# Kernel optimization log

Measured on AMD Instinct MI355X. Metric: run time of the kernel, lower is better.

## Reference

```python
import jax, jax.numpy as jnp
import numpy as np

N_USERS = 100_000
N_ITEMS = 50_000
N_NODES = N_USERS + N_ITEMS
D = 64
K = 32          # n_intents
N_LAYERS = 2
E_UI = 1_000_000
E_UU = 500_000
E_II = 500_000


def spmm(row, col, val, x, n_rows):
    # sparse[n_rows, :] @ x via gather + segment_sum  (torch_sparse.spmm)
    return jax.ops.segment_sum(val[:, None] * x[col], row, num_segments=n_rows)


def row_normalize(row, val, n_rows):
    # D^-1 * values, matching normalization_indices_values / embed21 row scaling
    s = jax.ops.segment_sum(val, row, num_segments=n_rows)
    inv = jnp.where(s != 0, 1.0 / s, 0.0)
    return inv[row] * val


def l2norm(x):
    # F.normalize(x) along dim=1
    return x / jnp.maximum(jnp.linalg.norm(x, axis=1, keepdims=True), 1e-12)


def setup_inputs():
    key = jax.random.key(0)
    ks = jax.random.split(key, 16)
    return dict(
        user_emb=0.1 * jax.random.normal(ks[0], (N_USERS, D), jnp.float32),
        item_emb=0.1 * jax.random.normal(ks[1], (N_ITEMS, D), jnp.float32),
        intents=0.1 * jax.random.normal(ks[2], (D, K), jnp.float32),
        W2=0.1 * jax.random.normal(ks[3], (4 * D, D), jnp.float32),
        b2=jnp.zeros((D,), jnp.float32),
        uu_w=jax.random.uniform(ks[4], (E_UU,), jnp.float32),
        ii_w=jax.random.uniform(ks[5], (E_II,), jnp.float32),
        ui_u=jax.random.randint(ks[6], (E_UI,), 0, N_USERS),
        ui_i=jax.random.randint(ks[7], (E_UI,), 0, N_ITEMS),
        uu_h=jax.random.randint(ks[8], (E_UU,), 0, N_USERS),
        uu_t=jax.random.randint(ks[9], (E_UU,), 0, N_USERS),
        ii_h=jax.random.randint(ks[10], (E_II,), 0, N_ITEMS),
        ii_t=jax.random.randint(ks[11], (E_II,), 0, N_ITEMS),
    )


def reference(user_emb, item_emb, intents, W2, b2, uu_w, ii_w,
              ui_u, ui_i, uu_h, uu_t, ii_h, ii_t):
    # symmetric bipartite adjacency: (u -> n_users+i) and (n_users+i -> u)
    all_h = jnp.concatenate([ui_u, ui_i + N_USERS])
    all_t = jnp.concatenate([ui_i + N_USERS, ui_u])

    # _cal_sparse_adj: G = D^-1/2 A D^-1/2 on edge values
    deg = jax.ops.segment_sum(jnp.ones((2 * E_UI,), jnp.float32), all_h,
                              num_segments=N_NODES)
    d_inv = jnp.where(deg > 0, deg ** -0.5, 0.0)
    G_val = d_inv[all_h] * d_inv[all_t]

    # normalization_indices_values for UU / II weighted graphs (D^-1 * w)
    uu_val = row_normalize(uu_h, uu_w, N_USERS)
    ii_val = row_normalize(ii_h, ii_w, N_ITEMS)

    def embed11(x):
        return spmm(all_h, all_t, G_val, x, N_NODES)

    def embed12(x):
        u, i = x[:N_USERS], x[N_USERS:]
        return jnp.concatenate([spmm(uu_h, uu_t, uu_val, u, N_USERS),
                                spmm(ii_h, ii_t, ii_val, i, N_ITEMS)], axis=0)

    def intent_edge_weights(h_emb, t_emb, head_idx, n_heads):
        # per-edge intent distribution + alpha-weighted node aggregation
        dist = jax.nn.softmax((h_emb * t_emb) @ intents, axis=1)   # [E, K]
        alpha = (jnp.sum(h_emb * t_emb, axis=1) + 1.0) / 2.0        # [E]
        agg = jax.ops.segment_sum(alpha[:, None] * dist, head_idx,
                                  num_segments=n_heads)             # [n, K]
        recip = jnp.where(agg != 0, 1.0 / agg, 0.0)
        edge_int = alpha[:, None] * recip[head_idx]                 # [E, K]
        return jnp.mean(dist * edge_int, axis=1)                    # [E]

    def embed21(feature, x):
        h = feature[ui_u]               # [E_UI, D]
        t = feature[ui_i + N_USERS]     # [E_UI, D]
        w_u = intent_edge_weights(h, t, ui_u, N_USERS)
        w_i = intent_edge_weights(h, t, ui_i, N_ITEMS)
        w = row_normalize(all_h, jnp.concatenate([w_u, w_i]), N_NODES)
        return l2norm(spmm(all_h, all_t, w, x, N_NODES))

    def embed22(feature, x):
        uf, itf = feature[:N_USERS], feature[N_USERS:]
        ux, ix = x[:N_USERS], x[N_USERS:]
        w_uu = intent_edge_weights(uf[uu_h], uf[uu_t], uu_h, N_USERS)
        w_uu = row_normalize(uu_h, w_uu, N_USERS)
        w_ii = intent_edge_weights(itf[ii_h], itf[ii_t], ii_h, N_ITEMS)
        w_ii = row_normalize(ii_h, w_ii, N_ITEMS)
        return l2norm(jnp.concatenate([spmm(uu_h, uu_t, w_uu, ux, N_USERS),
                                       spmm(ii_h, ii_t, w_ii, ix, N_ITEMS)], axis=0))

    x = jnp.concatenate([user_emb, item_emb], axis=0)
    acc = x
    for _ in range(N_LAYERS):
        g1 = embed11(x)
        g2 = embed12(x)
        t1 = embed21(x, x)
        t2 = embed22(x, x)
        # mlp2 fusion (eval mode, dropout off): sigmoid gate over 4-way concat
        gate = jax.nn.sigmoid(jnp.concatenate([g1, g2, t1, t2], axis=1) @ W2 + b2)
        x = gate * (g1 + g2) + (1.0 - gate) * (t1 + t2)
        acc = acc + x
    return acc
```

## Files before the change

kernel.cpp:

```cpp
#include <hip/hip_runtime.h>
#include <hip/hip_fp16.h>

#define NU 100000
#define NI 50000
#define NN 150000
#define DD 64
#define KK 32
#define EUI 1000000
#define EUU 500000
#define EII 500000
#define ROWS_PB 64

static inline int cdiv(long a, int b) { return (int)((a + b - 1) / b); }

__device__ __forceinline__ float rdlane(float v, int l) {
    return __int_as_float(__builtin_amdgcn_readlane(__float_as_int(v), l));
}


__global__ void k_count(const int* __restrict__ h, int* __restrict__ cnt, int E) {
    int e = blockIdx.x * blockDim.x + threadIdx.x;
    if (e < E) atomicAdd(&cnt[h[e]], 1);
}

__global__ __launch_bounds__(1024) void k_scan(const int* __restrict__ cnt,
                                               int* __restrict__ rp, int n) {
    __shared__ int wsum[16];
    __shared__ int carry_s;
    int tid = threadIdx.x;
    int lane = tid & 63, wid = tid >> 6;
    if (tid == 0) carry_s = 0;
    __syncthreads();
    for (int base = 0; base < n; base += 1024) {
        int i = base + tid;
        int v = (i < n) ? cnt[i] : 0;
        int s = v;
#pragma unroll
        for (int off = 1; off < 64; off <<= 1) {
            int t = __shfl_up(s, off, 64);
            if (lane >= off) s += t;
        }
        if (lane == 63) wsum[wid] = s;
        __syncthreads();
        int woff = 0, total = 0;
#pragma unroll
        for (int w = 0; w < 16; w++) { int ws = wsum[w]; total += ws; if (w < wid) woff += ws; }
        int carry = carry_s;
        if (i < n) rp[i] = carry + woff + (s - v);
        __syncthreads();
        if (tid == 0) carry_s = carry + total;
        __syncthreads();
    }
    if (tid == 0) rp[n] = carry_s;
}

__global__ void k_scatter(const int* __restrict__ h, const int* __restrict__ rp,
                          int* __restrict__ cur, int* __restrict__ lst, int E) {
    int e = blockIdx.x * blockDim.x + threadIdx.x;
    if (e >= E) return;
    int r = h[e];
    int p = rp[r] + atomicAdd(&cur[r], 1);
    lst[p] = e;
}

__global__ void k_dinv(const int* __restrict__ rpu, const int* __restrict__ rpi,
                       float* __restrict__ dinv) {
    int t = blockIdx.x * blockDim.x + threadIdx.x;
    if (t >= NN) return;
    int deg = (t < NU) ? rpu[t + 1] - rpu[t] : rpi[t - NU + 1] - rpi[t - NU];
    dinv[t] = deg > 0 ? rsqrtf((float)deg) : 0.0f;
}

__global__ void k_rowsum_inv(const int* __restrict__ rp, const int* __restrict__ lst,
                             const float* __restrict__ w, float* __restrict__ out, int n) {
    int r = blockIdx.x * blockDim.x + threadIdx.x;
    if (r >= n) return;
    float s = 0.f;
    int e1 = rp[r + 1];
    for (int e = rp[r]; e < e1; e++) s += w[lst[e]];
    out[r] = (s != 0.0f) ? 1.0f / s : 0.0f;
}

__global__ void k_wdiff(const float* __restrict__ W2, float* __restrict__ Wd_g,
                        float* __restrict__ Wd_t) {
    int i = blockIdx.x * blockDim.x + threadIdx.x;
    if (i >= DD * DD) return;
    Wd_g[i] = W2[i] - W2[DD * DD + i];
    Wd_t[i] = W2[2 * DD * DD + i] - W2[3 * DD * DD + i];
}

__global__ void k_init(const float* __restrict__ ue, const float* __restrict__ ie,
                       __half* __restrict__ xh, float* __restrict__ acc) {
    size_t i = (size_t)blockIdx.x * blockDim.x + threadIdx.x;
    if (i >= (size_t)NN * DD) return;
    float v = (i < (size_t)NU * DD) ? ue[i] : ie[i - (size_t)NU * DD];
    xh[i] = __float2half(v);
    acc[i] = v;
}


__global__ void k_posU(const int* __restrict__ lst, int* __restrict__ pos, int E) {
    int p = blockIdx.x * blockDim.x + threadIdx.x;
    if (p < E) pos[lst[p]] = p;
}

__global__ void k_mapUI(const int* __restrict__ lst_i, const int* __restrict__ posU,
                        int* __restrict__ mUI, int E) {
    int p = blockIdx.x * blockDim.x + threadIdx.x;
    if (p < E) mUI[p] = posU[lst_i[p]];
}

__global__ void k_build_ui(const int* __restrict__ lst_u, const int* __restrict__ ui_u,
                           const int* __restrict__ ui_i, int* __restrict__ headU,
                           int* __restrict__ colUI, int E) {
    int p = blockIdx.x * blockDim.x + threadIdx.x;
    if (p >= E) return;
    int e = lst_u[p];
    headU[p] = ui_u[e];
    colUI[p] = ui_i[e] + NU;
}

__global__ void k_build_colI(const int* __restrict__ lst_i, const int* __restrict__ ui_u,
                             int* __restrict__ colUI, int E) {
    int p = blockIdx.x * blockDim.x + threadIdx.x;
    if (p < E) colUI[EUI + p] = ui_u[lst_i[p]];
}

__global__ void k_build_rp2(const int* __restrict__ rp_u, const int* __restrict__ rp_i,
                            const int* __restrict__ rp_uu, const int* __restrict__ rp_ii,
                            int* __restrict__ rp_ui, int* __restrict__ rp_s) {
    int t = blockIdx.x * blockDim.x + threadIdx.x;
    if (t > NN) return;
    rp_ui[t] = (t <= NU) ? rp_u[t] : rp_i[t - NU] + EUI;
    rp_s[t]  = (t <= NU) ? rp_uu[t] : rp_ii[t - NU] + EUU;
}

__global__ void k_build_gw(const int* __restrict__ rp, const int* __restrict__ col,
                           const float* __restrict__ dinv, float* __restrict__ gw, int n) {
    int r = blockIdx.x * blockDim.x + threadIdx.x;
    if (r >= n) return;
    float dh = dinv[r];
    int e1 = rp[r + 1];
    for (int p = rp[r]; p < e1; p++) gw[p] = dh * dinv[col[p]];
}

__global__ void k_build_s(const int* __restrict__ lst, const int* __restrict__ eh,
                          const int* __restrict__ et, const float* __restrict__ ew,
                          const float* __restrict__ inv, int off, int peo,
                          int* __restrict__ head, int* __restrict__ col,
                          float* __restrict__ bw, int E) {
    int p = blockIdx.x * blockDim.x + threadIdx.x;
    if (p >= E) return;
    int e = lst[p];
    int h = eh[e];
    head[peo + p] = h + off;
    col[peo + p] = et[e] + off;
    bw[peo + p] = ew[e] * inv[h];
}


__global__ __launch_bounds__(256) void k_passA(
        const int* __restrict__ head, const int* __restrict__ col,
        const __half* __restrict__ x, const float* __restrict__ intents,
        __half* __restrict__ c_out, int E) {
    __shared__ float Wl[DD * KK];
    for (int idx = threadIdx.x; idx < DD * KK; idx += blockDim.x) Wl[idx] = intents[idx];
    __syncthreads();
    int stride = gridDim.x * blockDim.x;
    for (int p = blockIdx.x * blockDim.x + threadIdx.x; p < E; p += stride) {
        const uint4* hp = (const uint4*)(x + (size_t)head[p] * DD);
        const uint4* tp = (const uint4*)(x + (size_t)col[p] * DD);
        uint4 hraw[8], traw[8];
#pragma unroll
        for (int j = 0; j < 8; j++) hraw[j] = hp[j];
#pragma unroll
        for (int j = 0; j < 8; j++) traw[j] = tp[j];
        const __half2* h2 = (const __half2*)hraw;
        const __half2* t2 = (const __half2*)traw;
        float logit[KK];
#pragma unroll
        for (int k = 0; k < KK; k++) logit[k] = 0.f;
        float dot = 0.f;
#pragma unroll 4
        for (int l4 = 0; l4 < 16; l4++) {
            float2 ha = __half22float2(h2[2 * l4]), hb = __half22float2(h2[2 * l4 + 1]);
            float2 ta = __half22float2(t2[2 * l4]), tb = __half22float2(t2[2 * l4 + 1]);
            float p0 = ha.x * ta.x, p1 = ha.y * ta.y, p2 = hb.x * tb.x, p3 = hb.y * tb.y;
            dot += p0 + p1 + p2 + p3;
            const float* w = &Wl[l4 * 4 * KK];
#pragma unroll
            for (int k = 0; k < KK; k++)
                logit[k] += p0 * w[k] + p1 * w[KK + k] + p2 * w[2 * KK + k] + p3 * w[3 * KK + k];
        }
        float m = logit[0];
#pragma unroll
        for (int k = 1; k < KK; k++) m = fmaxf(m, logit[k]);
        float ssum = 0.f;
#pragma unroll
        for (int k = 0; k < KK; k++) { float ev = __expf(logit[k] - m); logit[k] = ev; ssum += ev; }
        float scale = 0.5f * (dot + 1.0f) / ssum;
        uint4 pk[4];
        unsigned int* u = (unsigned int*)pk;
#pragma unroll
        for (int k2 = 0; k2 < 16; k2++) {
            __half2 hh = __floats2half2_rn(logit[2 * k2] * scale, logit[2 * k2 + 1] * scale);
            u[k2] = *reinterpret_cast<const unsigned int*>(&hh);
        }
        uint4* dst = (uint4*)(c_out + (size_t)p * KK);
#pragma unroll
        for (int q = 0; q < 4; q++) dst[q] = pk[q];
    }
}

#define PRD(a0, a1, a2, a3, l) \
    rdlane(((l) & 3) == 0 ? (a0) : ((l) & 3) == 1 ? (a1) : ((l) & 3) == 2 ? (a2) : (a3), (l) >> 2)

__global__ __launch_bounds__(512) void k_fused_ui(
        const int* __restrict__ rp, const int* __restrict__ col,
        const float* __restrict__ gw, const __half* __restrict__ cbuf,
        const int* __restrict__ mUI,
        const float* __restrict__ Wd_g, const float* __restrict__ Wd_t,
        const float* __restrict__ b2, const __half* __restrict__ x,
        __half* __restrict__ gs, __half* __restrict__ ts,
        float* __restrict__ zp, int nrows) {
    __shared__ float Wg[DD * DD];
    __shared__ float Wt[DD * DD];
    for (int i = threadIdx.x; i < DD * DD; i += 512) { Wg[i] = Wd_g[i]; Wt[i] = Wd_t[i]; }
    __syncthreads();
    int wid = threadIdx.x >> 6, lane = threadIdx.x & 63;
    int sub = lane & 15, grp = lane >> 4;
    float b2v = b2[lane];
    const uint2* xq = (const uint2*)x;
    const unsigned int* cu = (const unsigned int*)cbuf;
    int rbase = blockIdx.x * ROWS_PB + wid * 8;
    for (int rr = 0; rr < 8; rr++) {
        int r = rbase + rr;
        if (r >= nrows) break;
        bool item = (r >= NU);
        int e0 = rp[r], e1 = rp[r + 1];
        float a0 = 0.f, a1 = 0.f;
        for (int e = e0; e < e1; e += 4) {
            int idx = e + grp;
            if (idx < e1) {
                int ci = item ? mUI[idx - EUI] : idx;
                unsigned int cv = cu[(size_t)ci * 16 + sub];
                float2 cf = __half22float2(*(const __half2*)&cv);
                a0 += cf.x; a1 += cf.y;
            }
        }
        a0 += __shfl_xor(a0, 16, 64); a0 += __shfl_xor(a0, 32, 64);
        a1 += __shfl_xor(a1, 16, 64); a1 += __shfl_xor(a1, 32, 64);
        float2 rc;
        rc.x = (a0 != 0.f) ? 1.f / a0 : 0.f;
        rc.y = (a1 != 0.f) ? 1.f / a1 : 0.f;
        float g0 = 0, g1 = 0, g2 = 0, g3 = 0, t0 = 0, t1 = 0, t2 = 0, t3 = 0;
        float rsacc = 0.f;
        int e = e0;
        for (; e + 8 <= e1; e += 8) {
#pragma unroll
            for (int u = 0; u < 2; u++) {
                int idx = e + 4 * u + grp;
                int cc = col[idx];
                float wg = gw[idx];
                int ci = item ? mUI[idx - EUI] : idx;
                unsigned int cv = cu[(size_t)ci * 16 + sub];
                float2 cf = __half22float2(*(const __half2*)&cv);
                float pd = fmaf(cf.x, rc.x, cf.y * rc.y);
                pd += __shfl_xor(pd, 1, 64); pd += __shfl_xor(pd, 2, 64);
                pd += __shfl_xor(pd, 4, 64); pd += __shfl_xor(pd, 8, 64);
                float wt = pd * (1.0f / KK);
                rsacc += wt;
                uint2 raw = xq[(size_t)cc * 16 + sub];
                float2 xa = __half22float2(*(const __half2*)&raw.x);
                float2 xb = __half22float2(*(const __half2*)&raw.y);
                g0 += wg * xa.x; g1 += wg * xa.y; g2 += wg * xb.x; g3 += wg * xb.y;
                t0 += wt * xa.x; t1 += wt * xa.y; t2 += wt * xb.x; t3 += wt * xb.y;
            }
        }
        for (; e < e1; e += 4) {
            int idx = e + grp;
            if (idx < e1) {
                int cc = col[idx];
                float wg = gw[idx];
                int ci = item ? mUI[idx - EUI] : idx;
                unsigned int cv = cu[(size_t)ci * 16 + sub];
                float2 cf = __half22float2(*(const __half2*)&cv);
                float pd = fmaf(cf.x, rc.x, cf.y * rc.y);
                pd += __shfl_xor(pd, 1, 64); pd += __shfl_xor(pd, 2, 64);
                pd += __shfl_xor(pd, 4, 64); pd += __shfl_xor(pd, 8, 64);
                float wt = pd * (1.0f / KK);
                rsacc += wt;
                uint2 raw = xq[(size_t)cc * 16 + sub];
                float2 xa = __half22float2(*(const __half2*)&raw.x);
                float2 xb = __half22float2(*(const __half2*)&raw.y);
                g0 += wg * xa.x; g1 += wg * xa.y; g2 += wg * xb.x; g3 += wg * xb.y;
                t0 += wt * xa.x; t1 += wt * xa.y; t2 += wt * xb.x; t3 += wt * xb.y;
            }
        }
#pragma unroll
        for (int off = 16; off <= 32; off <<= 1) {
            g0 += __shfl_xor(g0, off, 64); g1 += __shfl_xor(g1, off, 64);
            g2 += __shfl_xor(g2, off, 64); g3 += __shfl_xor(g3, off, 64);
            t0 += __shfl_xor(t0, off, 64); t1 += __shfl_xor(t1, off, 64);
            t2 += __shfl_xor(t2, off, 64); t3 += __shfl_xor(t3, off, 64);
            rsacc += __shfl_xor(rsacc, off, 64);
        }
        float rsv = (rsacc != 0.f) ? 1.0f / rsacc : 0.f;
        t0 *= rsv; t1 *= rsv; t2 *= rsv; t3 *= rsv;
        float ss = t0 * t0 + t1 * t1 + t2 * t2 + t3 * t3;
        ss += __shfl_xor(ss, 1, 64); ss += __shfl_xor(ss, 2, 64);
        ss += __shfl_xor(ss, 4, 64); ss += __shfl_xor(ss, 8, 64);
        float inv_n = 1.0f / fmaxf(sqrtf(ss), 1e-12f);
        t0 *= inv_n; t1 *= inv_n; t2 *= inv_n; t3 *= inv_n;
        float zv = b2v;
#pragma unroll
        for (int l = 0; l < DD; l++) {
            float gl = PRD(g0, g1, g2, g3, l);
            float tl = PRD(t0, t1, t2, t3, l);
            zv += gl * Wg[l * DD + lane] + tl * Wt[l * DD + lane];
        }
        float ga0 = __shfl(g0, lane >> 2, 64), ga1 = __shfl(g1, lane >> 2, 64);
        float ga2 = __shfl(g2, lane >> 2, 64), ga3 = __shfl(g3, lane >> 2, 64);
        float ta0 = __shfl(t0, lane >> 2, 64), ta1 = __shfl(t1, lane >> 2, 64);
        float ta2 = __shfl(t2, lane >> 2, 64), ta3 = __shfl(t3, lane >> 2, 64);
        int j = lane & 3;
        float gsv = j == 0 ? ga0 : j == 1 ? ga1 : j == 2 ? ga2 : ga3;
        float tsv = j == 0 ? ta0 : j == 1 ? ta1 : j == 2 ? ta2 : ta3;
        size_t oi = (size_t)r * DD + lane;
        gs[oi] = __float2half(gsv);
        ts[oi] = __float2half(tsv);
        zp[oi] = zv;
    }
}

__global__ __launch_bounds__(512) void k_fused_fin(
        const int* __restrict__ rp, const int* __restrict__ col,
        const float* __restrict__ bw, const __half* __restrict__ cbuf,
        const float* __restrict__ W1, const float* __restrict__ W3,
        const __half* __restrict__ x, const __half* __restrict__ gs,
        const __half* __restrict__ ts, const float* __restrict__ zp,
        __half* __restrict__ xh_out, float* __restrict__ acc, int nrows) {
    __shared__ float Wa[DD * DD];
    __shared__ float Wb[DD * DD];
    for (int i = threadIdx.x; i < DD * DD; i += 512) { Wa[i] = W1[i]; Wb[i] = W3[i]; }
    __syncthreads();
    int wid = threadIdx.x >> 6, lane = threadIdx.x & 63;
    int sub = lane & 15, grp = lane >> 4;
    const uint2* xq = (const uint2*)x;
    const unsigned int* cu = (const unsigned int*)cbuf;
    int rbase = blockIdx.x * ROWS_PB + wid * 8;
    for (int rr = 0; rr < 8; rr++) {
        int r = rbase + rr;
        if (r >= nrows) break;
        int e0 = rp[r], e1 = rp[r + 1];
        float a0 = 0.f, a1 = 0.f;
        for (int e = e0; e < e1; e += 4) {
            int idx = e + grp;
            if (idx < e1) {
                unsigned int cv = cu[(size_t)idx * 16 + sub];
                float2 cf = __half22float2(*(const __half2*)&cv);
                a0 += cf.x; a1 += cf.y;
            }
        }
        a0 += __shfl_xor(a0, 16, 64); a0 += __shfl_xor(a0, 32, 64);
        a1 += __shfl_xor(a1, 16, 64); a1 += __shfl_xor(a1, 32, 64);
        float2 rc;
        rc.x = (a0 != 0.f) ? 1.f / a0 : 0.f;
        rc.y = (a1 != 0.f) ? 1.f / a1 : 0.f;
        float g0 = 0, g1 = 0, g2 = 0, g3 = 0, t0 = 0, t1 = 0, t2 = 0, t3 = 0;
        float rsacc = 0.f;
        int e = e0;
        for (; e + 8 <= e1; e += 8) {
#pragma unroll
            for (int u = 0; u < 2; u++) {
                int idx = e + 4 * u + grp;
                int cc = col[idx];
                float wg = bw[idx];
                unsigned int cv = cu[(size_t)idx * 16 + sub];
                float2 cf = __half22float2(*(const __half2*)&cv);
                float pd = fmaf(cf.x, rc.x, cf.y * rc.y);
                pd += __shfl_xor(pd, 1, 64); pd += __shfl_xor(pd, 2, 64);
                pd += __shfl_xor(pd, 4, 64); pd += __shfl_xor(pd, 8, 64);
                float wt = pd * (1.0f / KK);
                rsacc += wt;
                uint2 raw = xq[(size_t)cc * 16 + sub];
                float2 xa = __half22float2(*(const __half2*)&raw.x);
                float2 xb = __half22float2(*(const __half2*)&raw.y);
                g0 += wg * xa.x; g1 += wg * xa.y; g2 += wg * xb.x; g3 += wg * xb.y;
                t0 += wt * xa.x; t1 += wt * xa.y; t2 += wt * xb.x; t3 += wt * xb.y;
            }
        }
        for (; e < e1; e += 4) {
            int idx = e + grp;
            if (idx < e1) {
                int cc = col[idx];
                float wg = bw[idx];
                unsigned int cv = cu[(size_t)idx * 16 + sub];
                float2 cf = __half22float2(*(const __half2*)&cv);
                float pd = fmaf(cf.x, rc.x, cf.y * rc.y);
                pd += __shfl_xor(pd, 1, 64); pd += __shfl_xor(pd, 2, 64);
                pd += __shfl_xor(pd, 4, 64); pd += __shfl_xor(pd, 8, 64);
                float wt = pd * (1.0f / KK);
                rsacc += wt;
                uint2 raw = xq[(size_t)cc * 16 + sub];
                float2 xa = __half22float2(*(const __half2*)&raw.x);
                float2 xb = __half22float2(*(const __half2*)&raw.y);
                g0 += wg * xa.x; g1 += wg * xa.y; g2 += wg * xb.x; g3 += wg * xb.y;
                t0 += wt * xa.x; t1 += wt * xa.y; t2 += wt * xb.x; t3 += wt * xb.y;
            }
        }
#pragma unroll
        for (int off = 16; off <= 32; off <<= 1) {
            g0 += __shfl_xor(g0, off, 64); g1 += __shfl_xor(g1, off, 64);
            g2 += __shfl_xor(g2, off, 64); g3 += __shfl_xor(g3, off, 64);
            t0 += __shfl_xor(t0, off, 64); t1 += __shfl_xor(t1, off, 64);
            t2 += __shfl_xor(t2, off, 64); t3 += __shfl_xor(t3, off, 64);
            rsacc += __shfl_xor(rsacc, off, 64);
        }
        float rsv = (rsacc != 0.f) ? 1.0f / rsacc : 0.f;
        t0 *= rsv; t1 *= rsv; t2 *= rsv; t3 *= rsv;
        float ss = t0 * t0 + t1 * t1 + t2 * t2 + t3 * t3;
        ss += __shfl_xor(ss, 1, 64); ss += __shfl_xor(ss, 2, 64);
        ss += __shfl_xor(ss, 4, 64); ss += __shfl_xor(ss, 8, 64);
        float inv_n = 1.0f / fmaxf(sqrtf(ss), 1e-12f);
        t0 *= inv_n; t1 *= inv_n; t2 *= inv_n; t3 *= inv_n;
        uint2 gp2 = ((const uint2*)(gs + (size_t)r * DD))[sub];
        uint2 tp2 = ((const uint2*)(ts + (size_t)r * DD))[sub];
        float2 gpa = __half22float2(*(const __half2*)&gp2.x);
        float2 gpb = __half22float2(*(const __half2*)&gp2.y);
        float2 tpa = __half22float2(*(const __half2*)&tp2.x);
        float2 tpb = __half22float2(*(const __half2*)&tp2.y);
        float gf0 = gpa.x + g0, gf1 = gpa.y + g1, gf2 = gpb.x + g2, gf3 = gpb.y + g3;
        float tf0 = tpa.x + t0, tf1 = tpa.y + t1, tf2 = tpb.x + t2, tf3 = tpb.y + t3;
        size_t oi = (size_t)r * DD + lane;
        float zv = zp[oi];
#pragma unroll
        for (int l = 0; l < DD; l++) {
            float gl = PRD(gf0, gf1, gf2, gf3, l);
            float tl = PRD(tf0, tf1, tf2, tf3, l);
            zv += gl * Wa[l * DD + lane] + tl * Wb[l * DD + lane];
        }
        float ga0 = __shfl(gf0, lane >> 2, 64), ga1 = __shfl(gf1, lane >> 2, 64);
        float ga2 = __shfl(gf2, lane >> 2, 64), ga3 = __shfl(gf3, lane >> 2, 64);
        float ta0 = __shfl(tf0, lane >> 2, 64), ta1 = __shfl(tf1, lane >> 2, 64);
        float ta2 = __shfl(tf2, lane >> 2, 64), ta3 = __shfl(tf3, lane >> 2, 64);
        int j = lane & 3;
        float gfin = j == 0 ? ga0 : j == 1 ? ga1 : j == 2 ? ga2 : ga3;
        float tfin = j == 0 ? ta0 : j == 1 ? ta1 : j == 2 ? ta2 : ta3;
        float gate = 1.0f / (1.0f + __expf(-zv));
        float xn = gate * gfin + (1.0f - gate) * tfin;
        xh_out[oi] = __float2half(xn);
        acc[oi] += xn;
    }
}


extern "C" void kernel_launch(void* const* d_in, const int* in_sizes, int n_in,
                              void* d_out, int out_size, void* d_ws, size_t ws_size,
                              hipStream_t stream) {
    const float* user_emb = (const float*)d_in[0];
    const float* item_emb = (const float*)d_in[1];
    const float* intents  = (const float*)d_in[2];
    const float* W2       = (const float*)d_in[3];
    const float* b2       = (const float*)d_in[4];
    const float* uu_w     = (const float*)d_in[5];
    const float* ii_w     = (const float*)d_in[6];
    const int*   ui_u     = (const int*)d_in[7];
    const int*   ui_i     = (const int*)d_in[8];
    const int*   uu_h     = (const int*)d_in[9];
    const int*   uu_t     = (const int*)d_in[10];
    const int*   ii_h     = (const int*)d_in[11];
    const int*   ii_t     = (const int*)d_in[12];
    float* acc = (float*)d_out;

    char* pw = (char*)d_ws;
    auto allocb = [&](size_t nbytes) -> char* {
        char* r = pw;
        pw += (nbytes + 255) & ~(size_t)255;
        return r;
    };
    __half* gs   = (__half*)allocb((size_t)NN * DD * 2);
    __half* ts   = (__half*)allocb((size_t)NN * DD * 2);
    float* zp    = (float*)allocb((size_t)NN * DD * 4);
    __half* xh0  = (__half*)allocb((size_t)NN * DD * 2);
    __half* xh1  = (__half*)allocb((size_t)NN * DD * 2);
    __half* c    = (__half*)allocb((size_t)EUI * KK * 2);
    float* dinv  = (float*)allocb((size_t)NN * 4);
    float* iuu   = (float*)allocb((size_t)NU * 4);
    float* iii   = (float*)allocb((size_t)NI * 4);
    float* Wd_g  = (float*)allocb((size_t)DD * DD * 4);
    float* Wd_t  = (float*)allocb((size_t)DD * DD * 4);
    int* rp_u    = (int*)allocb(((size_t)NU + 1) * 4);
    int* rp_i    = (int*)allocb(((size_t)NI + 1) * 4);
    int* rp_uu   = (int*)allocb(((size_t)NU + 1) * 4);
    int* rp_ii   = (int*)allocb(((size_t)NI + 1) * 4);
    int* rp_ui   = (int*)allocb(((size_t)NN + 1) * 4);
    int* rp_s    = (int*)allocb(((size_t)NN + 1) * 4);
    int* headU   = (int*)allocb((size_t)EUI * 4);
    int* colUI   = (int*)allocb((size_t)2 * EUI * 4);
    int* head_s  = (int*)allocb((size_t)(EUU + EII) * 4);
    int* col_s   = (int*)allocb((size_t)(EUU + EII) * 4);
    float* bw_s  = (float*)allocb((size_t)(EUU + EII) * 4);
    int* mUI     = (int*)allocb((size_t)EUI * 4);
    float* gwUI  = (float*)allocb((size_t)2 * EUI * 4);

    char* ca = (char*)c;
    int* cur    = (int*)ca;  ca += ((size_t)NU * 4 + 255) & ~(size_t)255;
    int* lst_u  = (int*)ca;  ca += ((size_t)EUI * 4 + 255) & ~(size_t)255;
    int* lst_i  = (int*)ca;  ca += ((size_t)EUI * 4 + 255) & ~(size_t)255;
    int* lst_uu = (int*)ca;  ca += ((size_t)EUU * 4 + 255) & ~(size_t)255;
    int* lst_ii = (int*)ca;  ca += ((size_t)EII * 4 + 255) & ~(size_t)255;
    int* posU   = (int*)ca;

    const int B = 256;

    auto build_csr = [&](const int* h, int E, int n, int* rp, int* lst) {
        hipMemsetAsync(cur, 0, (size_t)n * 4, stream);
        k_count<<<cdiv(E, B), B, 0, stream>>>(h, cur, E);
        k_scan<<<1, 1024, 0, stream>>>(cur, rp, n);
        hipMemsetAsync(cur, 0, (size_t)n * 4, stream);
        k_scatter<<<cdiv(E, B), B, 0, stream>>>(h, rp, cur, lst, E);
    };

    build_csr(ui_u, EUI, NU, rp_u, lst_u);
    build_csr(ui_i, EUI, NI, rp_i, lst_i);
    build_csr(uu_h, EUU, NU, rp_uu, lst_uu);
    build_csr(ii_h, EII, NI, rp_ii, lst_ii);
    k_dinv<<<cdiv(NN, B), B, 0, stream>>>(rp_u, rp_i, dinv);
    k_rowsum_inv<<<cdiv(NU, B), B, 0, stream>>>(rp_uu, lst_uu, uu_w, iuu, NU);
    k_rowsum_inv<<<cdiv(NI, B), B, 0, stream>>>(rp_ii, lst_ii, ii_w, iii, NI);
    k_build_rp2<<<cdiv(NN + 1, B), B, 0, stream>>>(rp_u, rp_i, rp_uu, rp_ii, rp_ui, rp_s);
    k_build_ui<<<cdiv(EUI, B), B, 0, stream>>>(lst_u, ui_u, ui_i, headU, colUI, EUI);
    k_build_colI<<<cdiv(EUI, B), B, 0, stream>>>(lst_i, ui_u, colUI, EUI);
    k_posU<<<cdiv(EUI, B), B, 0, stream>>>(lst_u, posU, EUI);
    k_mapUI<<<cdiv(EUI, B), B, 0, stream>>>(lst_i, posU, mUI, EUI);
    k_build_s<<<cdiv(EUU, B), B, 0, stream>>>(lst_uu, uu_h, uu_t, uu_w, iuu, 0, 0,
                                              head_s, col_s, bw_s, EUU);
    k_build_s<<<cdiv(EII, B), B, 0, stream>>>(lst_ii, ii_h, ii_t, ii_w, iii, NU, EUU,
                                              head_s, col_s, bw_s, EII);
    k_build_gw<<<cdiv(NN, B), B, 0, stream>>>(rp_ui, colUI, dinv, gwUI, NN);
    k_wdiff<<<cdiv(DD * DD, B), B, 0, stream>>>(W2, Wd_g, Wd_t);
    k_init<<<cdiv((long)NN * DD, B), B, 0, stream>>>(user_emb, item_emb, xh0, acc);

    for (int layer = 0; layer < 2; ++layer) {
        const __half* xin = (layer == 0) ? xh0 : xh1;
        __half* xout = (layer == 0) ? xh1 : xh0;

        k_passA<<<1024, B, 0, stream>>>(headU, colUI, xin, intents, c, EUI);
        k_fused_ui<<<cdiv(NN, ROWS_PB), 512, 0, stream>>>(rp_ui, colUI, gwUI, c, mUI,
                                                          Wd_g, Wd_t, b2, xin, gs, ts, zp, NN);

        k_passA<<<1024, B, 0, stream>>>(head_s, col_s, xin, intents, c, EUU + EII);
        k_fused_fin<<<cdiv(NN, ROWS_PB), 512, 0, stream>>>(rp_s, col_s, bw_s, c,
                                                           W2 + DD * DD, W2 + 3 * DD * DD,
                                                           xin, gs, ts, zp, xout, acc, NN);
    }
}
```

Before: 2.201 ms.

## Bucket edges by tail-node shard so passA gathers hit a localized x range

Adds a one-time counting sort that reorders each edge list into 8 shards by tail column range, with the original position kept for the output write. passA then assigns blocks to shards round-robin (blockIdx&7), so concurrently running blocks gather tail rows from a narrower slice of x, aiming for better L2/MALL locality on the random gathers. The cost is extra preprocessing kernels, extra index arrays, and scattered writes of the c output through tpos.

```diff
diff --git a/kernel.cpp b/kernel.cpp
--- a/kernel.cpp
+++ b/kernel.cpp
@@ -10,11 +10,17 @@
 #define EUU 500000
 #define EII 500000
 #define ROWS_PB 64
+#define NB_UI ((EUI + 255) / 256)
+#define NB_S ((EUU + EII + 255) / 256)
 
 static inline int cdiv(long a, int b) { return (int)((a + b - 1) / b); }
 
 __device__ __forceinline__ float rdlane(float v, int l) {
     return __int_as_float(__builtin_amdgcn_readlane(__float_as_int(v), l));
+}
+
+__device__ __forceinline__ int shard_of(int col) {
+    return (col < NU) ? col / 12500 : (col - NU) / 6250;
 }
 
 
@@ -159,17 +165,66 @@
 }
 
 
-__global__ __launch_bounds__(256) void k_passA(
+__global__ __launch_bounds__(256) void k_cntmat(const int* __restrict__ col,
+                                                int* __restrict__ cntmat, int NB, int E) {
+    __shared__ int lc[8];
+    if (threadIdx.x < 8) lc[threadIdx.x] = 0;
+    __syncthreads();
+    int p = blockIdx.x * 256 + threadIdx.x;
+    if (p < E) atomicAdd(&lc[shard_of(col[p])], 1);
+    __syncthreads();
+    if (threadIdx.x < 8) cntmat[threadIdx.x * NB + blockIdx.x] = lc[threadIdx.x];
+}
+
+__global__ __launch_bounds__(256) void k_scatmat(
         const int* __restrict__ head, const int* __restrict__ col,
+        const int* __restrict__ sc, int NB, int E,
+        int* __restrict__ head2, int* __restrict__ col2, int* __restrict__ tpos) {
+    __shared__ int sbase[8];
+    __shared__ int wcnt[4][8];
+    int tid = threadIdx.x, lane = tid & 63, w = tid >> 6;
+    if (tid < 8) sbase[tid] = sc[tid * NB + blockIdx.x];
+    int p = blockIdx.x * 256 + tid;
+    int sh = -1, h = 0, c = 0;
+    if (p < E) { h = head[p]; c = col[p]; sh = shard_of(c); }
+    int rank = 0;
+#pragma unroll
+    for (int s = 0; s < 8; s++) {
+        unsigned long long m = __ballot(sh == s);
+        if (sh == s) rank = __popcll(m & ((1ull << lane) - 1ull));
+        if (lane == 0) wcnt[w][s] = __popcll(m);
+    }
+    __syncthreads();
+    if (sh >= 0) {
+        int off = 0;
+#pragma unroll
+        for (int w2 = 0; w2 < 4; w2++) if (w2 < w) off += wcnt[w2][sh];
+        int pos = sbase[sh] + off + rank;
+        head2[pos] = h;
+        col2[pos] = c;
+        tpos[pos] = p;
+    }
+}
+
+
+__global__ __launch_bounds__(256) void k_passA_sh(
+        const int* __restrict__ head2, const int* __restrict__ col2,
+        const int* __restrict__ tpos, const int* __restrict__ sc, int NB, int E,
         const __half* __restrict__ x, const float* __restrict__ intents,
-        __half* __restrict__ c_out, int E) {
+        __half* __restrict__ c_out) {
     __shared__ float Wl[DD * KK];
     for (int idx = threadIdx.x; idx < DD * KK; idx += blockDim.x) Wl[idx] = intents[idx];
     __syncthreads();
-    int stride = gridDim.x * blockDim.x;
-    for (int p = blockIdx.x * blockDim.x + threadIdx.x; p < E; p += stride) {
-        const uint4* hp = (const uint4*)(x + (size_t)head[p] * DD);
-        const uint4* tp = (const uint4*)(x + (size_t)col[p] * DD);
+    int sh = blockIdx.x & 7;
+    int nchunk = gridDim.x >> 3;
+    int chunk0 = blockIdx.x >> 3;
+    int s0 = sc[sh * NB];
+    int s1 = sc[(sh + 1) * NB];
+    for (int base = s0 + chunk0 * 256; base < s1; base += nchunk * 256) {
+        int p2 = base + threadIdx.x;
+        if (p2 >= s1) continue;
+        const uint4* hp = (const uint4*)(x + (size_t)head2[p2] * DD);
+        const uint4* tp = (const uint4*)(x + (size_t)col2[p2] * DD);
         uint4 hraw[8], traw[8];
 #pragma unroll
         for (int j = 0; j < 8; j++) hraw[j] = hp[j];
@@ -185,12 +240,12 @@
         for (int l4 = 0; l4 < 16; l4++) {
             float2 ha = __half22float2(h2[2 * l4]), hb = __half22float2(h2[2 * l4 + 1]);
             float2 ta = __half22float2(t2[2 * l4]), tb = __half22float2(t2[2 * l4 + 1]);
-            float p0 = ha.x * ta.x, p1 = ha.y * ta.y, p2 = hb.x * tb.x, p3 = hb.y * tb.y;
-            dot += p0 + p1 + p2 + p3;
+            float p0 = ha.x * ta.x, p1 = ha.y * ta.y, p2f = hb.x * tb.x, p3 = hb.y * tb.y;
+            dot += p0 + p1 + p2f + p3;
             const float* w = &Wl[l4 * 4 * KK];
 #pragma unroll
             for (int k = 0; k < KK; k++)
-                logit[k] += p0 * w[k] + p1 * w[KK + k] + p2 * w[2 * KK + k] + p3 * w[3 * KK + k];
+                logit[k] += p0 * w[k] + p1 * w[KK + k] + p2f * w[2 * KK + k] + p3 * w[3 * KK + k];
         }
         float m = logit[0];
 #pragma unroll
@@ -206,7 +261,7 @@
             __half2 hh = __floats2half2_rn(logit[2 * k2] * scale, logit[2 * k2 + 1] * scale);
             u[k2] = *reinterpret_cast<const unsigned int*>(&hh);
         }
-        uint4* dst = (uint4*)(c_out + (size_t)p * KK);
+        uint4* dst = (uint4*)(c_out + (size_t)tpos[p2] * KK);
 #pragma unroll
         for (int q = 0; q < 4; q++) dst[q] = pk[q];
     }
@@ -503,6 +558,14 @@
     float* bw_s  = (float*)allocb((size_t)(EUU + EII) * 4);
     int* mUI     = (int*)allocb((size_t)EUI * 4);
     float* gwUI  = (float*)allocb((size_t)2 * EUI * 4);
+    int* scU     = (int*)allocb((size_t)(8 * NB_UI + 1) * 4);
+    int* scS     = (int*)allocb((size_t)(8 * NB_S + 1) * 4);
+    int* h2U     = (int*)allocb((size_t)EUI * 4);
+    int* c2U     = (int*)allocb((size_t)EUI * 4);
+    int* tpU     = (int*)allocb((size_t)EUI * 4);
+    int* h2S     = (int*)allocb((size_t)(EUU + EII) * 4);
+    int* c2S     = (int*)allocb((size_t)(EUU + EII) * 4);
+    int* tpS     = (int*)allocb((size_t)(EUU + EII) * 4);
 
     char* ca = (char*)c;
     int* cur    = (int*)ca;  ca += ((size_t)NU * 4 + 255) & ~(size_t)255;
@@ -510,7 +573,9 @@
     int* lst_i  = (int*)ca;  ca += ((size_t)EUI * 4 + 255) & ~(size_t)255;
     int* lst_uu = (int*)ca;  ca += ((size_t)EUU * 4 + 255) & ~(size_t)255;
     int* lst_ii = (int*)ca;  ca += ((size_t)EII * 4 + 255) & ~(size_t)255;
-    int* posU   = (int*)ca;
+    int* posU   = (int*)ca;  ca += ((size_t)EUI * 4 + 255) & ~(size_t)255;
+    int* cmU    = (int*)ca;  ca += ((size_t)(8 * NB_UI) * 4 + 255) & ~(size_t)255;
+    int* cmS    = (int*)ca;
 
     const int B = 256;
 
@@ -542,15 +607,22 @@
     k_wdiff<<<cdiv(DD * DD, B), B, 0, stream>>>(W2, Wd_g, Wd_t);
     k_init<<<cdiv((long)NN * DD, B), B, 0, stream>>>(user_emb, item_emb, xh0, acc);
 
+    k_cntmat<<<NB_UI, B, 0, stream>>>(colUI, cmU, NB_UI, EUI);
+    k_scan<<<1, 1024, 0, stream>>>(cmU, scU, 8 * NB_UI);
+    k_scatmat<<<NB_UI, B, 0, stream>>>(headU, colUI, scU, NB_UI, EUI, h2U, c2U, tpU);
+    k_cntmat<<<NB_S, B, 0, stream>>>(col_s, cmS, NB_S, EUU + EII);
+    k_scan<<<1, 1024, 0, stream>>>(cmS, scS, 8 * NB_S);
+    k_scatmat<<<NB_S, B, 0, stream>>>(head_s, col_s, scS, NB_S, EUU + EII, h2S, c2S, tpS);
+
     for (int layer = 0; layer < 2; ++layer) {
         const __half* xin = (layer == 0) ? xh0 : xh1;
         __half* xout = (layer == 0) ? xh1 : xh0;
 
-        k_passA<<<1024, B, 0, stream>>>(headU, colUI, xin, intents, c, EUI);
+        k_passA_sh<<<2048, B, 0, stream>>>(h2U, c2U, tpU, scU, NB_UI, EUI, xin, intents, c);
         k_fused_ui<<<cdiv(NN, ROWS_PB), 512, 0, stream>>>(rp_ui, colUI, gwUI, c, mUI,
                                                           Wd_g, Wd_t, b2, xin, gs, ts, zp, NN);
 
-        k_passA<<<1024, B, 0, stream>>>(head_s, col_s, xin, intents, c, EUU + EII);
+        k_passA_sh<<<2048, B, 0, stream>>>(h2S, c2S, tpS, scS, NB_S, EUU + EII, xin, intents, c);
         k_fused_fin<<<cdiv(NN, ROWS_PB), 512, 0, stream>>>(rp_s, col_s, bw_s, c,
                                                            W2 + DD * DD, W2 + 3 * DD * DD,
                                                            xin, gs, ts, zp, xout, acc, NN);
```

After: 2.323 ms. +5.5%, slower.

## Merge UI aggregation with UU/II intent pass and store intents as FP8

Applied to the files above, without the earlier changes.

Combines the UI fused aggregation and the UU/II intent-weight pass into one kernel whose blocks take roles by blockIdx modulo 3, so the two independent stages run concurrently and one launch goes away. The UU/II intent coefficients are now written into a separate buffer in a custom 8-bit E4M3-style encoding with software encode/decode, which halves their write and read traffic in k_fused_fin. In exchange, intent weights lose precision, the encode/decode adds ALU work, and the mixed-role kernel keeps the larger shared-memory footprint for every block, which may limit occupancy.

```diff
diff --git a/kernel.cpp b/kernel.cpp
--- a/kernel.cpp
+++ b/kernel.cpp
@@ -10,11 +10,35 @@
 #define EUU 500000
 #define EII 500000
 #define ROWS_PB 64
+#define FB 2344
+#define PB 1172
+#define MEGA_GRID (FB + PB)
 
 static inline int cdiv(long a, int b) { return (int)((a + b - 1) / b); }
 
 __device__ __forceinline__ float rdlane(float v, int l) {
     return __int_as_float(__builtin_amdgcn_readlane(__float_as_int(v), l));
+}
+
+__device__ __forceinline__ unsigned int enc8(float f) {
+    float a = fabsf(f) * 32.0f;
+    unsigned int s = (__float_as_uint(f) >> 31) << 7;
+    if (a < 0.015625f) return s;
+    if (a > 448.0f) a = 448.0f;
+    unsigned int ub = __float_as_uint(a);
+    ub += 0x7FFFF + ((ub >> 20) & 1);
+    int ex = (int)((ub >> 23) & 0xff) - 127;
+    if (ex < -6) return s;
+    unsigned int m = (ub >> 20) & 7;
+    unsigned int e = (unsigned int)(ex + 7);
+    if (e > 15) { e = 15; m = 7; }
+    return s | (e << 3) | m;
+}
+__device__ __forceinline__ float dec8(unsigned int b) {
+    unsigned int s = (b >> 7) & 1, e = (b >> 3) & 15, m = b & 7;
+    if ((b & 0x7f) == 0) return 0.f;
+    unsigned int ub = ((e + 120) << 23) | (m << 20) | (s << 31);
+    return __uint_as_float(ub) * 0.03125f;
 }
 
 
@@ -215,127 +239,184 @@
 #define PRD(a0, a1, a2, a3, l) \
     rdlane(((l) & 3) == 0 ? (a0) : ((l) & 3) == 1 ? (a1) : ((l) & 3) == 2 ? (a2) : (a3), (l) >> 2)
 
-__global__ __launch_bounds__(512) void k_fused_ui(
+__global__ __launch_bounds__(512) void k_mega(
         const int* __restrict__ rp, const int* __restrict__ col,
         const float* __restrict__ gw, const __half* __restrict__ cbuf,
         const int* __restrict__ mUI,
         const float* __restrict__ Wd_g, const float* __restrict__ Wd_t,
         const float* __restrict__ b2, const __half* __restrict__ x,
-        __half* __restrict__ gs, __half* __restrict__ ts,
-        float* __restrict__ zp, int nrows) {
-    __shared__ float Wg[DD * DD];
-    __shared__ float Wt[DD * DD];
-    for (int i = threadIdx.x; i < DD * DD; i += 512) { Wg[i] = Wd_g[i]; Wt[i] = Wd_t[i]; }
-    __syncthreads();
-    int wid = threadIdx.x >> 6, lane = threadIdx.x & 63;
-    int sub = lane & 15, grp = lane >> 4;
-    float b2v = b2[lane];
-    const uint2* xq = (const uint2*)x;
-    const unsigned int* cu = (const unsigned int*)cbuf;
-    int rbase = blockIdx.x * ROWS_PB + wid * 8;
-    for (int rr = 0; rr < 8; rr++) {
-        int r = rbase + rr;
-        if (r >= nrows) break;
-        bool item = (r >= NU);
-        int e0 = rp[r], e1 = rp[r + 1];
-        float a0 = 0.f, a1 = 0.f;
-        for (int e = e0; e < e1; e += 4) {
-            int idx = e + grp;
-            if (idx < e1) {
-                int ci = item ? mUI[idx - EUI] : idx;
-                unsigned int cv = cu[(size_t)ci * 16 + sub];
-                float2 cf = __half22float2(*(const __half2*)&cv);
-                a0 += cf.x; a1 += cf.y;
-            }
-        }
-        a0 += __shfl_xor(a0, 16, 64); a0 += __shfl_xor(a0, 32, 64);
-        a1 += __shfl_xor(a1, 16, 64); a1 += __shfl_xor(a1, 32, 64);
-        float2 rc;
-        rc.x = (a0 != 0.f) ? 1.f / a0 : 0.f;
-        rc.y = (a1 != 0.f) ? 1.f / a1 : 0.f;
-        float g0 = 0, g1 = 0, g2 = 0, g3 = 0, t0 = 0, t1 = 0, t2 = 0, t3 = 0;
-        float rsacc = 0.f;
-        int e = e0;
-        for (; e + 8 <= e1; e += 8) {
-#pragma unroll
-            for (int u = 0; u < 2; u++) {
-                int idx = e + 4 * u + grp;
-                int cc = col[idx];
-                float wg = gw[idx];
-                int ci = item ? mUI[idx - EUI] : idx;
-                unsigned int cv = cu[(size_t)ci * 16 + sub];
-                float2 cf = __half22float2(*(const __half2*)&cv);
-                float pd = fmaf(cf.x, rc.x, cf.y * rc.y);
-                pd += __shfl_xor(pd, 1, 64); pd += __shfl_xor(pd, 2, 64);
-                pd += __shfl_xor(pd, 4, 64); pd += __shfl_xor(pd, 8, 64);
-                float wt = pd * (1.0f / KK);
-                rsacc += wt;
-                uint2 raw = xq[(size_t)cc * 16 + sub];
-                float2 xa = __half22float2(*(const __half2*)&raw.x);
-                float2 xb = __half22float2(*(const __half2*)&raw.y);
-                g0 += wg * xa.x; g1 += wg * xa.y; g2 += wg * xb.x; g3 += wg * xb.y;
-                t0 += wt * xa.x; t1 += wt * xa.y; t2 += wt * xb.x; t3 += wt * xb.y;
-            }
-        }
-        for (; e < e1; e += 4) {
-            int idx = e + grp;
-            if (idx < e1) {
-                int cc = col[idx];
-                float wg = gw[idx];
-                int ci = item ? mUI[idx - EUI] : idx;
-                unsigned int cv = cu[(size_t)ci * 16 + sub];
-                float2 cf = __half22float2(*(const __half2*)&cv);
-                float pd = fmaf(cf.x, rc.x, cf.y * rc.y);
-                pd += __shfl_xor(pd, 1, 64); pd += __shfl_xor(pd, 2, 64);
-                pd += __shfl_xor(pd, 4, 64); pd += __shfl_xor(pd, 8, 64);
-                float wt = pd * (1.0f / KK);
-                rsacc += wt;
-                uint2 raw = xq[(size_t)cc * 16 + sub];
-                float2 xa = __half22float2(*(const __half2*)&raw.x);
-                float2 xb = __half22float2(*(const __half2*)&raw.y);
-                g0 += wg * xa.x; g1 += wg * xa.y; g2 += wg * xb.x; g3 += wg * xb.y;
-                t0 += wt * xa.x; t1 += wt * xa.y; t2 += wt * xb.x; t3 += wt * xb.y;
-            }
-        }
-#pragma unroll
-        for (int off = 16; off <= 32; off <<= 1) {
-            g0 += __shfl_xor(g0, off, 64); g1 += __shfl_xor(g1, off, 64);
-            g2 += __shfl_xor(g2, off, 64); g3 += __shfl_xor(g3, off, 64);
-            t0 += __shfl_xor(t0, off, 64); t1 += __shfl_xor(t1, off, 64);
-            t2 += __shfl_xor(t2, off, 64); t3 += __shfl_xor(t3, off, 64);
-            rsacc += __shfl_xor(rsacc, off, 64);
-        }
-        float rsv = (rsacc != 0.f) ? 1.0f / rsacc : 0.f;
-        t0 *= rsv; t1 *= rsv; t2 *= rsv; t3 *= rsv;
-        float ss = t0 * t0 + t1 * t1 + t2 * t2 + t3 * t3;
-        ss += __shfl_xor(ss, 1, 64); ss += __shfl_xor(ss, 2, 64);
-        ss += __shfl_xor(ss, 4, 64); ss += __shfl_xor(ss, 8, 64);
-        float inv_n = 1.0f / fmaxf(sqrtf(ss), 1e-12f);
-        t0 *= inv_n; t1 *= inv_n; t2 *= inv_n; t3 *= inv_n;
-        float zv = b2v;
-#pragma unroll
-        for (int l = 0; l < DD; l++) {
-            float gl = PRD(g0, g1, g2, g3, l);
-            float tl = PRD(t0, t1, t2, t3, l);
-            zv += gl * Wg[l * DD + lane] + tl * Wt[l * DD + lane];
-        }
-        float ga0 = __shfl(g0, lane >> 2, 64), ga1 = __shfl(g1, lane >> 2, 64);
-        float ga2 = __shfl(g2, lane >> 2, 64), ga3 = __shfl(g3, lane >> 2, 64);
-        float ta0 = __shfl(t0, lane >> 2, 64), ta1 = __shfl(t1, lane >> 2, 64);
-        float ta2 = __shfl(t2, lane >> 2, 64), ta3 = __shfl(t3, lane >> 2, 64);
-        int j = lane & 3;
-        float gsv = j == 0 ? ga0 : j == 1 ? ga1 : j == 2 ? ga2 : ga3;
-        float tsv = j == 0 ? ta0 : j == 1 ? ta1 : j == 2 ? ta2 : ta3;
-        size_t oi = (size_t)r * DD + lane;
-        gs[oi] = __float2half(gsv);
-        ts[oi] = __float2half(tsv);
-        zp[oi] = zv;
+        __half* __restrict__ gs, __half* __restrict__ ts, float* __restrict__ zp,
+        const int* __restrict__ head_s, const int* __restrict__ col_s,
+        const float* __restrict__ intents, unsigned char* __restrict__ c8) {
+    __shared__ float shmem[2 * DD * DD];
+    int role = blockIdx.x % 3;
+    if (role < 2) {
+        float* Wg = shmem;
+        float* Wt = shmem + DD * DD;
+        for (int i = threadIdx.x; i < DD * DD; i += 512) { Wg[i] = Wd_g[i]; Wt[i] = Wd_t[i]; }
+        __syncthreads();
+        int fb = (blockIdx.x / 3) * 2 + role;
+        int wid = threadIdx.x >> 6, lane = threadIdx.x & 63;
+        int sub = lane & 15, grp = lane >> 4;
+        float b2v = b2[lane];
+        const uint2* xq = (const uint2*)x;
+        const unsigned int* cu = (const unsigned int*)cbuf;
+        int rbase = fb * ROWS_PB + wid * 8;
+        for (int rr = 0; rr < 8; rr++) {
+            int r = rbase + rr;
+            if (r >= NN) break;
+            bool item = (r >= NU);
+            int e0 = rp[r], e1 = rp[r + 1];
+            float a0 = 0.f, a1 = 0.f;
+            for (int e = e0; e < e1; e += 4) {
+                int idx = e + grp;
+                if (idx < e1) {
+                    int ci = item ? mUI[idx - EUI] : idx;
+                    unsigned int cv = cu[(size_t)ci * 16 + sub];
+                    float2 cf = __half22float2(*(const __half2*)&cv);
+                    a0 += cf.x; a1 += cf.y;
+                }
+            }
+            a0 += __shfl_xor(a0, 16, 64); a0 += __shfl_xor(a0, 32, 64);
+            a1 += __shfl_xor(a1, 16, 64); a1 += __shfl_xor(a1, 32, 64);
+            float2 rc;
+            rc.x = (a0 != 0.f) ? 1.f / a0 : 0.f;
+            rc.y = (a1 != 0.f) ? 1.f / a1 : 0.f;
+            float g0 = 0, g1 = 0, g2 = 0, g3 = 0, t0 = 0, t1 = 0, t2 = 0, t3 = 0;
+            float rsacc = 0.f;
+            int e = e0;
+            for (; e + 8 <= e1; e += 8) {
+#pragma unroll
+                for (int u = 0; u < 2; u++) {
+                    int idx = e + 4 * u + grp;
+                    int cc = col[idx];
+                    float wg = gw[idx];
+                    int ci = item ? mUI[idx - EUI] : idx;
+                    unsigned int cv = cu[(size_t)ci * 16 + sub];
+                    float2 cf = __half22float2(*(const __half2*)&cv);
+                    float pd = fmaf(cf.x, rc.x, cf.y * rc.y);
+                    pd += __shfl_xor(pd, 1, 64); pd += __shfl_xor(pd, 2, 64);
+                    pd += __shfl_xor(pd, 4, 64); pd += __shfl_xor(pd, 8, 64);
+                    float wt = pd * (1.0f / KK);
+                    rsacc += wt;
+                    uint2 raw = xq[(size_t)cc * 16 + sub];
+                    float2 xa = __half22float2(*(const __half2*)&raw.x);
+                    float2 xb = __half22float2(*(const __half2*)&raw.y);
+                    g0 += wg * xa.x; g1 += wg * xa.y; g2 += wg * xb.x; g3 += wg * xb.y;
+                    t0 += wt * xa.x; t1 += wt * xa.y; t2 += wt * xb.x; t3 += wt * xb.y;
+                }
+            }
+            for (; e < e1; e += 4) {
+                int idx = e + grp;
+                if (idx < e1) {
+                    int cc = col[idx];
+                    float wg = gw[idx];
+                    int ci = item ? mUI[idx - EUI] : idx;
+                    unsigned int cv = cu[(size_t)ci * 16 + sub];
+                    float2 cf = __half22float2(*(const __half2*)&cv);
+                    float pd = fmaf(cf.x, rc.x, cf.y * rc.y);
+                    pd += __shfl_xor(pd, 1, 64); pd += __shfl_xor(pd, 2, 64);
+                    pd += __shfl_xor(pd, 4, 64); pd += __shfl_xor(pd, 8, 64);
+                    float wt = pd * (1.0f / KK);
+                    rsacc += wt;
+                    uint2 raw = xq[(size_t)cc * 16 + sub];
+                    float2 xa = __half22float2(*(const __half2*)&raw.x);
+                    float2 xb = __half22float2(*(const __half2*)&raw.y);
+                    g0 += wg * xa.x; g1 += wg * xa.y; g2 += wg * xb.x; g3 += wg * xb.y;
+                    t0 += wt * xa.x; t1 += wt * xa.y; t2 += wt * xb.x; t3 += wt * xb.y;
+                }
+            }
+#pragma unroll
+            for (int off = 16; off <= 32; off <<= 1) {
+                g0 += __shfl_xor(g0, off, 64); g1 += __shfl_xor(g1, off, 64);
+                g2 += __shfl_xor(g2, off, 64); g3 += __shfl_xor(g3, off, 64);
+                t0 += __shfl_xor(t0, off, 64); t1 += __shfl_xor(t1, off, 64);
+                t2 += __shfl_xor(t2, off, 64); t3 += __shfl_xor(t3, off, 64);
+                rsacc += __shfl_xor(rsacc, off, 64);
+            }
+            float rsv = (rsacc != 0.f) ? 1.0f / rsacc : 0.f;
+            t0 *= rsv; t1 *= rsv; t2 *= rsv; t3 *= rsv;
+            float ss = t0 * t0 + t1 * t1 + t2 * t2 + t3 * t3;
+            ss += __shfl_xor(ss, 1, 64); ss += __shfl_xor(ss, 2, 64);
+            ss += __shfl_xor(ss, 4, 64); ss += __shfl_xor(ss, 8, 64);
+            float inv_n = 1.0f / fmaxf(sqrtf(ss), 1e-12f);
+            t0 *= inv_n; t1 *= inv_n; t2 *= inv_n; t3 *= inv_n;
+            float zv = b2v;
+#pragma unroll
+            for (int l = 0; l < DD; l++) {
+                float gl = PRD(g0, g1, g2, g3, l);
+                float tl = PRD(t0, t1, t2, t3, l);
+                zv += gl * Wg[l * DD + lane] + tl * Wt[l * DD + lane];
+            }
+            float ga0 = __shfl(g0, lane >> 2, 64), ga1 = __shfl(g1, lane >> 2, 64);
+            float ga2 = __shfl(g2, lane >> 2, 64), ga3 = __shfl(g3, lane >> 2, 64);
+            float ta0 = __shfl(t0, lane >> 2, 64), ta1 = __shfl(t1, lane >> 2, 64);
+            float ta2 = __shfl(t2, lane >> 2, 64), ta3 = __shfl(t3, lane >> 2, 64);
+            int j = lane & 3;
+            float gsv = j == 0 ? ga0 : j == 1 ? ga1 : j == 2 ? ga2 : ga3;
+            float tsv = j == 0 ? ta0 : j == 1 ? ta1 : j == 2 ? ta2 : ta3;
+            size_t oi = (size_t)r * DD + lane;
+            gs[oi] = __float2half(gsv);
+            ts[oi] = __float2half(tsv);
+            zp[oi] = zv;
+        }
+    } else {
+        float* Wl = shmem;
+        for (int idx = threadIdx.x; idx < DD * KK; idx += 512) Wl[idx] = intents[idx];
+        __syncthreads();
+        int pb = blockIdx.x / 3;
+        const int ES = EUU + EII;
+        int stride = PB * 512;
+        for (int p = pb * 512 + threadIdx.x; p < ES; p += stride) {
+            const uint4* hp = (const uint4*)(x + (size_t)head_s[p] * DD);
+            const uint4* tp = (const uint4*)(x + (size_t)col_s[p] * DD);
+            uint4 hraw[8], traw[8];
+#pragma unroll
+            for (int j = 0; j < 8; j++) hraw[j] = hp[j];
+#pragma unroll
+            for (int j = 0; j < 8; j++) traw[j] = tp[j];
+            const __half2* h2 = (const __half2*)hraw;
+            const __half2* t2 = (const __half2*)traw;
+            float logit[KK];
+#pragma unroll
+            for (int k = 0; k < KK; k++) logit[k] = 0.f;
+            float dot = 0.f;
+#pragma unroll 4
+            for (int l4 = 0; l4 < 16; l4++) {
+                float2 ha = __half22float2(h2[2 * l4]), hb = __half22float2(h2[2 * l4 + 1]);
+                float2 ta = __half22float2(t2[2 * l4]), tb = __half22float2(t2[2 * l4 + 1]);
+                float p0 = ha.x * ta.x, p1 = ha.y * ta.y, p2 = hb.x * tb.x, p3 = hb.y * tb.y;
+                dot += p0 + p1 + p2 + p3;
+                const float* w = &Wl[l4 * 4 * KK];
+#pragma unroll
+                for (int k = 0; k < KK; k++)
+                    logit[k] += p0 * w[k] + p1 * w[KK + k] + p2 * w[2 * KK + k] + p3 * w[3 * KK + k];
+            }
+            float m = logit[0];
+#pragma unroll
+            for (int k = 1; k < KK; k++) m = fmaxf(m, logit[k]);
+            float ssum = 0.f;
+#pragma unroll
+            for (int k = 0; k < KK; k++) { float ev = __expf(logit[k] - m); logit[k] = ev; ssum += ev; }
+            float scale = 0.5f * (dot + 1.0f) / ssum;
+            unsigned int w8[8];
+#pragma unroll
+            for (int q = 0; q < 8; q++) {
+                w8[q] = enc8(logit[4 * q] * scale)
+                      | (enc8(logit[4 * q + 1] * scale) << 8)
+                      | (enc8(logit[4 * q + 2] * scale) << 16)
+                      | (enc8(logit[4 * q + 3] * scale) << 24);
+            }
+            uint4* dst = (uint4*)(c8 + (size_t)p * 32);
+            dst[0] = make_uint4(w8[0], w8[1], w8[2], w8[3]);
+            dst[1] = make_uint4(w8[4], w8[5], w8[6], w8[7]);
+        }
     }
 }
 
 __global__ __launch_bounds__(512) void k_fused_fin(
         const int* __restrict__ rp, const int* __restrict__ col,
-        const float* __restrict__ bw, const __half* __restrict__ cbuf,
+        const float* __restrict__ bw, const unsigned char* __restrict__ c8,
         const float* __restrict__ W1, const float* __restrict__ W3,
         const __half* __restrict__ x, const __half* __restrict__ gs,
         const __half* __restrict__ ts, const float* __restrict__ zp,
@@ -347,7 +428,7 @@
     int wid = threadIdx.x >> 6, lane = threadIdx.x & 63;
     int sub = lane & 15, grp = lane >> 4;
     const uint2* xq = (const uint2*)x;
-    const unsigned int* cu = (const unsigned int*)cbuf;
+    const unsigned short* cs = (const unsigned short*)c8;
     int rbase = blockIdx.x * ROWS_PB + wid * 8;
     for (int rr = 0; rr < 8; rr++) {
         int r = rbase + rr;
@@ -357,9 +438,8 @@
         for (int e = e0; e < e1; e += 4) {
             int idx = e + grp;
             if (idx < e1) {
-                unsigned int cv = cu[(size_t)idx * 16 + sub];
-                float2 cf = __half22float2(*(const __half2*)&cv);
-                a0 += cf.x; a1 += cf.y;
+                unsigned int cv = cs[(size_t)idx * 16 + sub];
+                a0 += dec8(cv & 0xff); a1 += dec8(cv >> 8);
             }
         }
         a0 += __shfl_xor(a0, 16, 64); a0 += __shfl_xor(a0, 32, 64);
@@ -376,9 +456,9 @@
                 int idx = e + 4 * u + grp;
                 int cc = col[idx];
                 float wg = bw[idx];
-                unsigned int cv = cu[(size_t)idx * 16 + sub];
-                float2 cf = __half22float2(*(const __half2*)&cv);
-                float pd = fmaf(cf.x, rc.x, cf.y * rc.y);
+                unsigned int cv = cs[(size_t)idx * 16 + sub];
+                float cx = dec8(cv & 0xff), cy = dec8(cv >> 8);
+                float pd = fmaf(cx, rc.x, cy * rc.y);
                 pd += __shfl_xor(pd, 1, 64); pd += __shfl_xor(pd, 2, 64);
                 pd += __shfl_xor(pd, 4, 64); pd += __shfl_xor(pd, 8, 64);
                 float wt = pd * (1.0f / KK);
@@ -395,9 +475,9 @@
             if (idx < e1) {
                 int cc = col[idx];
                 float wg = bw[idx];
-                unsigned int cv = cu[(size_t)idx * 16 + sub];
-                float2 cf = __half22float2(*(const __half2*)&cv);
-                float pd = fmaf(cf.x, rc.x, cf.y * rc.y);
+                unsigned int cv = cs[(size_t)idx * 16 + sub];
+                float cx = dec8(cv & 0xff), cy = dec8(cv >> 8);
+                float pd = fmaf(cx, rc.x, cy * rc.y);
                 pd += __shfl_xor(pd, 1, 64); pd += __shfl_xor(pd, 2, 64);
                 pd += __shfl_xor(pd, 4, 64); pd += __shfl_xor(pd, 8, 64);
                 float wt = pd * (1.0f / KK);
@@ -485,6 +565,7 @@
     __half* xh0  = (__half*)allocb((size_t)NN * DD * 2);
     __half* xh1  = (__half*)allocb((size_t)NN * DD * 2);
     __half* c    = (__half*)allocb((size_t)EUI * KK * 2);
+    unsigned char* c8 = (unsigned char*)allocb((size_t)(EUU + EII) * KK);
     float* dinv  = (float*)allocb((size_t)NN * 4);
     float* iuu   = (float*)allocb((size_t)NU * 4);
     float* iii   = (float*)allocb((size_t)NI * 4);
@@ -547,12 +628,11 @@
         __half* xout = (layer == 0) ? xh1 : xh0;
 
         k_passA<<<1024, B, 0, stream>>>(headU, colUI, xin, intents, c, EUI);
-        k_fused_ui<<<cdiv(NN, ROWS_PB), 512, 0, stream>>>(rp_ui, colUI, gwUI, c, mUI,
-                                                          Wd_g, Wd_t, b2, xin, gs, ts, zp, NN);
-
-        k_passA<<<1024, B, 0, stream>>>(head_s, col_s, xin, intents, c, EUU + EII);
-        k_fused_fin<<<cdiv(NN, ROWS_PB), 512, 0, stream>>>(rp_s, col_s, bw_s, c,
-                                                           W2 + DD * DD, W2 + 3 * DD * DD,
-                                                           xin, gs, ts, zp, xout, acc, NN);
+        k_mega<<<MEGA_GRID, 512, 0, stream>>>(rp_ui, colUI, gwUI, c, mUI,
+                                              Wd_g, Wd_t, b2, xin, gs, ts, zp,
+                                              head_s, col_s, intents, c8);
+        k_fused_fin<<<FB, 512, 0, stream>>>(rp_s, col_s, bw_s, c8,
+                                            W2 + DD * DD, W2 + 3 * DD * DD,
+                                            xin, gs, ts, zp, xout, acc, NN);
     }
 }
```

Measured after the change: 2.295 ms. 4.2% more time.
